# Kernel optimization log

Hardware: AMD Instinct MI355X
Metric: run time of the kernel (lower is better)

Reference implementation:

```python
import jax, jax.numpy as jnp
import numpy as np

N_NODES = 50000
N_EDGES = 800000
NODE_F = 64
HID = 64
LSTM_F = 32
LSTM_H = 128
B = 64
T = 200
OUT = 1
N_LAYERS = 2


def setup_inputs() -> dict:
    key = jax.random.key(0)
    ks = jax.random.split(key, 16)
    s = 0.05
    return {
        "x": jax.random.normal(ks[0], (N_NODES, NODE_F), jnp.float32),
        "edge_attr": jax.random.normal(ks[1], (N_EDGES, NODE_F), jnp.float32),
        "x_seq": jax.random.normal(ks[2], (B, T, LSTM_F), jnp.float32),
        "lin_W": jax.random.normal(ks[3], (N_LAYERS, HID, HID), jnp.float32) * s,
        "lin_b": jnp.zeros((N_LAYERS, HID), jnp.float32),
        "mlp_W1": jax.random.normal(ks[4], (N_LAYERS, HID, HID), jnp.float32) * s,
        "mlp_b1": jnp.zeros((N_LAYERS, HID), jnp.float32),
        "mlp_W2": jax.random.normal(ks[5], (N_LAYERS, HID, HID), jnp.float32) * s,
        "mlp_b2": jnp.zeros((N_LAYERS, HID), jnp.float32),
        "eps": jnp.zeros((N_LAYERS,), jnp.float32),
        "ln_scale": jnp.ones((N_LAYERS, HID), jnp.float32),
        "ln_bias": jnp.zeros((N_LAYERS, HID), jnp.float32),
        "W_ih": jax.random.normal(ks[6], (4 * LSTM_H, HID + LSTM_F), jnp.float32) * s,
        "W_hh": jax.random.normal(ks[7], (4 * LSTM_H, LSTM_H), jnp.float32) * s,
        "b_ih": jnp.zeros((4 * LSTM_H,), jnp.float32),
        "b_hh": jnp.zeros((4 * LSTM_H,), jnp.float32),
        "lstm_ln_scale": jnp.ones((LSTM_H,), jnp.float32),
        "lstm_ln_bias": jnp.zeros((LSTM_H,), jnp.float32),
        "fc_W": jax.random.normal(ks[8], (OUT, LSTM_H), jnp.float32) * s,
        "fc_b": jnp.zeros((OUT,), jnp.float32),
        "edge_index": jax.random.randint(ks[9], (2, N_EDGES), 0, N_NODES, jnp.int32),
        "node_indices": jax.random.randint(ks[10], (B,), 0, N_NODES, jnp.int32),
    }


def _layernorm(z, scale, bias, eps=1e-5):
    mu = jnp.mean(z, axis=-1, keepdims=True)
    var = jnp.var(z, axis=-1, keepdims=True)
    return (z - mu) * jax.lax.rsqrt(var + eps) * scale + bias


def reference(x, edge_attr, x_seq, lin_W, lin_b, mlp_W1, mlp_b1, mlp_W2, mlp_b2,
              eps, ln_scale, ln_bias, W_ih, W_hh, b_ih, b_hh,
              lstm_ln_scale, lstm_ln_bias, fc_W, fc_b, edge_index, node_indices):
    src, dst = edge_index[0], edge_index[1]
    h = x
    n = x.shape[0]
    # GINEConv layers: out = MLP((1+eps)*x + sum_j relu(x_j + lin(e_ij)))
    for l in range(N_LAYERS):
        e = edge_attr @ lin_W[l].T + lin_b[l]            # [E, C]
        m = jax.nn.relu(h[src] + e)                       # gather + message
        agg = jax.ops.segment_sum(m, dst, num_segments=n) # scatter-add
        z = (1.0 + eps[l]) * h + agg
        z = jax.nn.relu(z @ mlp_W1[l].T + mlp_b1[l]) @ mlp_W2[l].T + mlp_b2[l]
        z = _layernorm(z, ln_scale[l], ln_bias[l])
        h = jax.nn.relu(z)

    sel = h[node_indices]                                 # [B, HID]
    seq_len = x_seq.shape[1]
    expanded = jnp.broadcast_to(sel[:, None, :], (sel.shape[0], seq_len, sel.shape[1]))
    combined = jnp.concatenate([expanded, x_seq], axis=2) # [B, T, HID+F]

    # single-layer LSTM, PyTorch gate order (i, f, g, o)
    Hd = W_hh.shape[1]
    xs = jnp.transpose(combined, (1, 0, 2))               # [T, B, D]
    x_proj = xs @ W_ih.T + b_ih                            # [T, B, 4H]

    def step(carry, xp):
        hprev, cprev = carry
        gates = xp + hprev @ W_hh.T + b_hh
        i, f, g, o = jnp.split(gates, 4, axis=-1)
        i = jax.nn.sigmoid(i); f = jax.nn.sigmoid(f)
        g = jnp.tanh(g); o = jax.nn.sigmoid(o)
        c = f * cprev + i * g
        hn = o * jnp.tanh(c)
        return (hn, c), None

    bsz = combined.shape[0]
    init = (jnp.zeros((bsz, Hd), combined.dtype), jnp.zeros((bsz, Hd), combined.dtype))
    (hn, _), _ = jax.lax.scan(step, init, x_proj)

    last = _layernorm(hn, lstm_ln_scale, lstm_ln_bias)
    return last @ fc_W.T + fc_b
```

## Files before the change

### kernel.cpp

```cpp
#include <hip/hip_runtime.h>
#include <cmath>

static constexpr int NN  = 50000;
static constexpr int NE  = 800000;
static constexpr int HID = 64;
static constexpr int BB  = 64;
static constexpr int TT  = 200;
static constexpr int LH  = 128;
static constexpr int G4  = 512;

static constexpr int SCB = 125;
static constexpr int SCH = 400;

typedef _Float16 h2 __attribute__((ext_vector_type(2)));

#ifndef __has_builtin
#define __has_builtin(x) 0
#endif
#if __has_builtin(__builtin_amdgcn_fdot2)
__device__ __forceinline__ float fdot2_(h2 a, h2 b, float c) {
    return __builtin_amdgcn_fdot2(a, b, c, false);
}
#else
__device__ __forceinline__ float fdot2_(h2 a, h2 b, float c) {
    return c + (float)a.x * (float)b.x + (float)a.y * (float)b.y;
}
#endif

__device__ __forceinline__ h2 as_h2(unsigned int u) {
    union { unsigned int u; h2 h; } cv; cv.u = u; return cv.h;
}
__device__ __forceinline__ unsigned int as_u32(h2 h) {
    union { h2 h; unsigned int u; } cv; cv.h = h; return cv.u;
}

__device__ __forceinline__ float sigmoid_fast(float x) {
    return __fdividef(1.f, 1.f + __expf(-x));
}
__device__ __forceinline__ float tanh_fast(float x) {
    return __fdividef(2.f, 1.f + __expf(-2.f * x)) - 1.f;
}

__global__ __launch_bounds__(256) void hist_kernel(const int* __restrict__ dsts,
                                                   int* __restrict__ deg) {
    int i = blockIdx.x * 256 + threadIdx.x;
    if (i < NE) atomicAdd(&deg[dsts[i]], 1);
}

__global__ __launch_bounds__(512) void scan1_kernel(const int* __restrict__ deg,
                                                    int* __restrict__ loc,
                                                    int* __restrict__ bsum) {
    __shared__ int ws[8];
    const int b = blockIdx.x, t = threadIdx.x;
    const int idx = b * SCH + t;
    const int lane = t & 63, wv = t >> 6;
    int v = (t < SCH && idx < NN) ? deg[idx] : 0;
    int x = v;
    #pragma unroll
    for (int off = 1; off < 64; off <<= 1) {
        int y = __shfl_up(x, off);
        if (lane >= off) x += y;
    }
    if (lane == 63) ws[wv] = x;
    __syncthreads();
    if (t < 8) {
        int s = ws[t];
        #pragma unroll
        for (int off = 1; off < 8; off <<= 1) {
            int y = __shfl_up(s, off);
            if (t >= off) s += y;
        }
        ws[t] = s;
    }
    __syncthreads();
    const int base = wv ? ws[wv - 1] : 0;
    if (t < SCH && idx < NN) loc[idx] = base + x - v;
    if (t == 511) bsum[b] = ws[7];
}

__global__ void scan2_kernel(const int* __restrict__ bsum,
                             int* __restrict__ boff,
                             int* __restrict__ rowptr) {
    int tot = 0;
    for (int i = 0; i < SCB; ++i) { boff[i] = tot; tot += bsum[i]; }
    rowptr[NN] = tot;
}

__global__ __launch_bounds__(512) void scan3_kernel(const int* __restrict__ loc,
                                                    const int* __restrict__ boff,
                                                    int* __restrict__ rowptr,
                                                    int* __restrict__ head) {
    const int b = blockIdx.x, t = threadIdx.x;
    const int idx = b * SCH + t;
    if (t < SCH && idx < NN) {
        int r = loc[idx] + boff[b];
        rowptr[idx] = r;
        head[idx] = r;
    }
}

__global__ __launch_bounds__(256) void scatter_kernel(const int* __restrict__ srcs,
                                                      const int* __restrict__ dsts,
                                                      int* __restrict__ head,
                                                      int* __restrict__ perm,
                                                      int* __restrict__ ssrc) {
    int e = blockIdx.x * 256 + threadIdx.x;
    if (e < NE) {
        int d = dsts[e];
        int pos = atomicAdd(&head[d], 1);
        perm[e] = pos;
        ssrc[pos] = srcs[e];
    }
}

__global__ __launch_bounds__(256) void permute_kernel(const float* __restrict__ ea,
                                                      const int* __restrict__ perm,
                                                      ushort4* __restrict__ easort) {
    const int lane = threadIdx.x & 63, wid = threadIdx.x >> 6;
    const int slot = lane >> 4, hw = lane & 15;
    const int e = (blockIdx.x * 4 + wid) * 4 + slot;
    if (e < NE) {
        const int p = perm[e];
        float4 v = ((const float4*)ea)[(size_t)e * 16 + hw];
        union { _Float16 h[4]; ushort4 u; } pk;
        pk.h[0] = (_Float16)v.x; pk.h[1] = (_Float16)v.y;
        pk.h[2] = (_Float16)v.z; pk.h[3] = (_Float16)v.w;
        easort[(size_t)p * 16 + hw] = pk.u;
    }
}

__global__ __launch_bounds__(256) void edge_agg_kernel(
    const float*   __restrict__ h_in,
    const ushort4* __restrict__ easort,
    const float*   __restrict__ W,
    const float*   __restrict__ bias,
    const int*     __restrict__ rowptr,
    const int*     __restrict__ ssrc,
    float*         __restrict__ agg)
{
    __shared__ ushort4 stage[4][64];
    const int lane = threadIdx.x & 63;
    const int wid  = threadIdx.x >> 6;
    const int slot = lane >> 4, hw = lane & 15;

    h2 w2[32];
    {
        const float4* wf = (const float4*)(W + lane * 64);
        #pragma unroll
        for (int k4 = 0; k4 < 16; ++k4) {
            float4 v = wf[k4];
            h2 a; a.x = (_Float16)v.x; a.y = (_Float16)v.y;
            h2 b; b.x = (_Float16)v.z; b.y = (_Float16)v.w;
            w2[2*k4] = a; w2[2*k4+1] = b;
        }
    }
    const float bc = bias[lane];

    const int gw = blockIdx.x * 4 + wid;
    const int nw = gridDim.x * 4;
    for (int n = gw; n < NN; n += nw) {
        const int ofs = rowptr[n];
        const int dg  = rowptr[n + 1] - ofs;
        float acc = 0.f;
        for (int c = 0; c < dg; c += 4) {
            const int rem = dg - c;
            const int pick = slot < rem ? slot : rem - 1;
            const int ssv = ssrc[ofs + c + pick];
            stage[wid][lane] = easort[(size_t)(ofs + c + pick) * 16 + hw];
            if (rem >= 4) {
                float hv[4];
                #pragma unroll
                for (int j = 0; j < 4; ++j) {
                    int sj = __shfl(ssv, j << 4);
                    hv[j] = h_in[(size_t)sj * HID + lane];
                }
                asm volatile("s_waitcnt lgkmcnt(0)" ::: "memory");
                #pragma unroll
                for (int j = 0; j < 4; ++j) {
                    const uint4* stu = (const uint4*)&stage[wid][j * 16];
                    float aE = bc;
                    #pragma unroll
                    for (int k = 0; k < 8; ++k) {
                        uint4 u = stu[k];
                        aE = fdot2_(as_h2(u.x), w2[4*k+0], aE);
                        aE = fdot2_(as_h2(u.y), w2[4*k+1], aE);
                        aE = fdot2_(as_h2(u.z), w2[4*k+2], aE);
                        aE = fdot2_(as_h2(u.w), w2[4*k+3], aE);
                    }
                    float m = aE + hv[j];
                    acc += m > 0.f ? m : 0.f;
                }
            } else {
                asm volatile("s_waitcnt lgkmcnt(0)" ::: "memory");
                for (int j = 0; j < rem; ++j) {
                    int sj = __shfl(ssv, j << 4);
                    const uint4* stu = (const uint4*)&stage[wid][j * 16];
                    float aE = bc;
                    #pragma unroll
                    for (int k = 0; k < 8; ++k) {
                        uint4 u = stu[k];
                        aE = fdot2_(as_h2(u.x), w2[4*k+0], aE);
                        aE = fdot2_(as_h2(u.y), w2[4*k+1], aE);
                        aE = fdot2_(as_h2(u.z), w2[4*k+2], aE);
                        aE = fdot2_(as_h2(u.w), w2[4*k+3], aE);
                    }
                    float m = aE + h_in[(size_t)sj * HID + lane];
                    acc += m > 0.f ? m : 0.f;
                }
            }
        }
        agg[(size_t)n * HID + lane] = acc;
    }
}

__global__ __launch_bounds__(256) void node_kernel(
    const float* __restrict__ h_in,
    const float* __restrict__ agg,
    const float* __restrict__ W1, const float* __restrict__ b1,
    const float* __restrict__ W2, const float* __restrict__ b2,
    const float* __restrict__ epsp,
    const float* __restrict__ lnS, const float* __restrict__ lnB,
    float*       __restrict__ h_out)
{
    __shared__ float zbuf[4][64];
    __shared__ float tbuf[4][64];
    const int lane = threadIdx.x & 63;
    const int wid  = threadIdx.x >> 6;

    float w1[64], w2[64];
    {
        const float4* wf1 = (const float4*)(W1 + lane * 64);
        const float4* wf2 = (const float4*)(W2 + lane * 64);
        #pragma unroll
        for (int k4 = 0; k4 < 16; ++k4) {
            float4 a = wf1[k4], b = wf2[k4];
            w1[4*k4+0]=a.x; w1[4*k4+1]=a.y; w1[4*k4+2]=a.z; w1[4*k4+3]=a.w;
            w2[4*k4+0]=b.x; w2[4*k4+1]=b.y; w2[4*k4+2]=b.z; w2[4*k4+3]=b.w;
        }
    }
    const float b1c = b1[lane], b2c = b2[lane];
    const float sC = lnS[lane], bC = lnB[lane];
    const float epv = 1.f + epsp[0];

    const int gw = blockIdx.x * 4 + wid;
    const int nw = gridDim.x * 4;
    for (int n = gw; n < NN; n += nw) {
        float z = epv * h_in[(size_t)n*HID + lane] + agg[(size_t)n*HID + lane];
        zbuf[wid][lane] = z;
        asm volatile("s_waitcnt lgkmcnt(0)" ::: "memory");
        float acc = b1c;
        {
            const float4* zf = (const float4*)&zbuf[wid][0];
            #pragma unroll
            for (int k4 = 0; k4 < 16; ++k4) {
                float4 v = zf[k4];
                acc = fmaf(v.x, w1[4*k4+0], acc);
                acc = fmaf(v.y, w1[4*k4+1], acc);
                acc = fmaf(v.z, w1[4*k4+2], acc);
                acc = fmaf(v.w, w1[4*k4+3], acc);
            }
        }
        acc = acc > 0.f ? acc : 0.f;
        tbuf[wid][lane] = acc;
        asm volatile("s_waitcnt lgkmcnt(0)" ::: "memory");
        float acc2 = b2c;
        {
            const float4* tf = (const float4*)&tbuf[wid][0];
            #pragma unroll
            for (int k4 = 0; k4 < 16; ++k4) {
                float4 v = tf[k4];
                acc2 = fmaf(v.x, w2[4*k4+0], acc2);
                acc2 = fmaf(v.y, w2[4*k4+1], acc2);
                acc2 = fmaf(v.z, w2[4*k4+2], acc2);
                acc2 = fmaf(v.w, w2[4*k4+3], acc2);
            }
        }
        float s1 = acc2, s2 = acc2 * acc2;
        #pragma unroll
        for (int off = 32; off >= 1; off >>= 1) {
            s1 += __shfl_xor(s1, off);
            s2 += __shfl_xor(s2, off);
        }
        float mu  = s1 * (1.f/64.f);
        float var = s2 * (1.f/64.f) - mu * mu;
        float r   = rsqrtf(var + 1e-5f);
        float o   = (acc2 - mu) * r * sC + bC;
        h_out[(size_t)n*HID + lane] = o > 0.f ? o : 0.f;
    }
}

__global__ __launch_bounds__(512) void prep_kernel(
    const float* __restrict__ Wih,
    const float* __restrict__ bih,
    const float* __restrict__ h2v,
    const int*   __restrict__ nidx,
    float*       __restrict__ W2T,
    float*       __restrict__ selp)
{
    const int g = threadIdx.x;
    const int pos = ((g & 127) << 2) | (g >> 7);
    if (blockIdx.x == BB) {
        #pragma unroll
        for (int k = 0; k < 32; ++k)
            W2T[k * G4 + pos] = Wih[g * 96 + 64 + k];
    } else {
        const int b = blockIdx.x;
        __shared__ float hrow[64];
        if (g < 64) hrow[g] = h2v[(size_t)nidx[b] * HID + g];
        __syncthreads();
        float acc = bih[g];
        #pragma unroll
        for (int k = 0; k < 64; ++k)
            acc = fmaf(hrow[k], Wih[g * 96 + k], acc);
        selp[b * G4 + pos] = acc;
    }
}

__global__ __launch_bounds__(512) void xp_kernel(
    const float* __restrict__ xseq,
    const float* __restrict__ selp,
    const float* __restrict__ W2T,
    float*       __restrict__ xp)
{
    const int g   = threadIdx.x;
    const int row = blockIdx.x;
    const int t   = row >> 6;
    const int b   = row & 63;
    __shared__ float xs[32];
    if (g < 32) xs[g] = xseq[((size_t)b * TT + t) * 32 + g];
    __syncthreads();
    float acc = selp[b * G4 + g];
    #pragma unroll
    for (int k = 0; k < 32; ++k)
        acc = fmaf(xs[k], W2T[k * G4 + g], acc);
    xp[(size_t)row * G4 + g] = acc;
}

__global__ __launch_bounds__(512) void lstm_kernel(
    const float* __restrict__ xp,
    const float* __restrict__ Whh,
    const float* __restrict__ bhh,
    const float* __restrict__ lnS, const float* __restrict__ lnB,
    const float* __restrict__ fcW,
    const float* __restrict__ fcb,
    float*       __restrict__ out)
{
    const int t  = threadIdx.x;
    const int b  = blockIdx.x;
    const int gt = t & 3;
    const int j  = t >> 2;
    const int gate = gt * LH + j;

    h2 w2[64];
    {
        const float4* wf = (const float4*)(Whh + (size_t)gate * LH);
        #pragma unroll
        for (int k4 = 0; k4 < 32; ++k4) {
            float4 v = wf[k4];
            h2 a; a.x = (_Float16)v.x; a.y = (_Float16)v.y;
            h2 c2; c2.x = (_Float16)v.z; c2.y = (_Float16)v.w;
            w2[2*k4] = a; w2[2*k4+1] = c2;
        }
    }
    const float bg = bhh[gate];
    const float s_ = (gt == 2) ? 2.f : 1.f;
    const float a_ = (gt == 2) ? 2.f : 1.f;
    const float d_ = (gt == 2) ? -1.f : 0.f;

    __shared__ unsigned int h2b0[64];
    __shared__ unsigned int h2b1[64];
    __shared__ float h_final[LH];
    if (t < 64) h2b0[t] = 0u;
    float c = 0.f;
    __syncthreads();

    float xv = xp[(size_t)b * G4 + t];

    auto step = [&](const unsigned int* hb, unsigned int* hw, int ts) {
        const int tn = (ts + 1 < TT) ? ts + 1 : ts;
        const float xv_next = xp[((size_t)tn * BB + b) * G4 + t];

        float a0 = 0.f, a1 = 0.f, a2 = 0.f, a3 = 0.f;
        const uint4* hb4 = (const uint4*)hb;
        #pragma unroll
        for (int k = 0; k < 16; k += 4) {
            uint4 u0 = hb4[k], u1 = hb4[k+1], u2 = hb4[k+2], u3 = hb4[k+3];
            a0 = fdot2_(as_h2(u0.x), w2[4*k+ 0], a0);
            a0 = fdot2_(as_h2(u0.y), w2[4*k+ 1], a0);
            a0 = fdot2_(as_h2(u0.z), w2[4*k+ 2], a0);
            a0 = fdot2_(as_h2(u0.w), w2[4*k+ 3], a0);
            a1 = fdot2_(as_h2(u1.x), w2[4*k+ 4], a1);
            a1 = fdot2_(as_h2(u1.y), w2[4*k+ 5], a1);
            a1 = fdot2_(as_h2(u1.z), w2[4*k+ 6], a1);
            a1 = fdot2_(as_h2(u1.w), w2[4*k+ 7], a1);
            a2 = fdot2_(as_h2(u2.x), w2[4*k+ 8], a2);
            a2 = fdot2_(as_h2(u2.y), w2[4*k+ 9], a2);
            a2 = fdot2_(as_h2(u2.z), w2[4*k+10], a2);
            a2 = fdot2_(as_h2(u2.w), w2[4*k+11], a2);
            a3 = fdot2_(as_h2(u3.x), w2[4*k+12], a3);
            a3 = fdot2_(as_h2(u3.y), w2[4*k+13], a3);
            a3 = fdot2_(as_h2(u3.z), w2[4*k+14], a3);
            a3 = fdot2_(as_h2(u3.w), w2[4*k+15], a3);
        }
        float acc = xv + bg + ((a0 + a1) + (a2 + a3));

        float act = fmaf(a_, __fdividef(1.f, 1.f + __expf(-s_ * acc)), d_);

        float v0 = act;
        float v1 = __shfl_xor(v0, 1);
        float v2 = __shfl_xor(v0, 2);
        float v3 = __shfl_xor(v1, 2);
        float iv = (gt==0)?v0:(gt==1)?v1:(gt==2)?v2:v3;
        float fv = (gt==1)?v0:(gt==0)?v1:(gt==3)?v2:v3;
        float gv = (gt==2)?v0:(gt==3)?v1:(gt==0)?v2:v3;
        float ov = (gt==3)?v0:(gt==2)?v1:(gt==1)?v2:v3;

        c = fmaf(fv, c, iv * gv);
        float hval = ov * tanh_fast(c);

        float hpart = __shfl_xor(hval, 4);
        if ((t & 7) == 0) {
            h2 p; p.x = (_Float16)hval; p.y = (_Float16)hpart;
            hw[j >> 1] = as_u32(p);
        }
        if (gt == 0) h_final[j] = hval;
        __syncthreads();

        xv = xv_next;
    };

    for (int ts = 0; ts < TT; ts += 2) {
        step(h2b0, h2b1, ts);
        step(h2b1, h2b0, ts + 1);
    }

    if (t < 64) {
        float h0 = h_final[t], h1 = h_final[t + 64];
        float s1 = h0 + h1, s2 = h0*h0 + h1*h1;
        #pragma unroll
        for (int off = 32; off >= 1; off >>= 1) {
            s1 += __shfl_xor(s1, off);
            s2 += __shfl_xor(s2, off);
        }
        float mu  = s1 * (1.f/128.f);
        float var = s2 * (1.f/128.f) - mu * mu;
        float r   = rsqrtf(var + 1e-5f);
        float p = ((h0 - mu)*r*lnS[t]      + lnB[t])      * fcW[t]
                + ((h1 - mu)*r*lnS[t + 64] + lnB[t + 64]) * fcW[t + 64];
        #pragma unroll
        for (int off = 32; off >= 1; off >>= 1) p += __shfl_xor(p, off);
        if (t == 0) out[b] = p + fcb[0];
    }
}

extern "C" void kernel_launch(void* const* d_in, const int* in_sizes, int n_in,
                              void* d_out, int out_size, void* d_ws, size_t ws_size,
                              hipStream_t stream) {
    const float* x     = (const float*)d_in[0];
    const float* ea    = (const float*)d_in[1];
    const float* xseq  = (const float*)d_in[2];
    const float* linW  = (const float*)d_in[3];
    const float* linB  = (const float*)d_in[4];
    const float* mW1   = (const float*)d_in[5];
    const float* mb1   = (const float*)d_in[6];
    const float* mW2   = (const float*)d_in[7];
    const float* mb2   = (const float*)d_in[8];
    const float* eps   = (const float*)d_in[9];
    const float* lnS   = (const float*)d_in[10];
    const float* lnB   = (const float*)d_in[11];
    const float* Wih   = (const float*)d_in[12];
    const float* Whh   = (const float*)d_in[13];
    const float* bih   = (const float*)d_in[14];
    const float* bhh   = (const float*)d_in[15];
    const float* llnS  = (const float*)d_in[16];
    const float* llnB  = (const float*)d_in[17];
    const float* fcW   = (const float*)d_in[18];
    const float* fcb   = (const float*)d_in[19];
    const int*   eidx  = (const int*)d_in[20];
    const int*   nidx  = (const int*)d_in[21];
    float* out = (float*)d_out;

    const int* srcs = eidx;
    const int* dsts = eidx + NE;

    float* ws   = (float*)d_ws;
    float* agg  = ws;
    float* h1   = agg  + (size_t)NN * HID;
    float* h2m  = h1   + (size_t)NN * HID;
    float* selp = h2m  + (size_t)NN * HID;
    float* W2T  = selp + (size_t)BB * G4;
    float* xp   = W2T  + (size_t)32 * G4;
    int*   deg    = (int*)(xp + (size_t)TT * BB * G4);
    int*   rowptr = deg + NN;
    int*   head   = rowptr + NN + 2;
    int*   loc    = head + NN;
    int*   bsum   = loc + NN;
    int*   boff   = bsum + SCB + 3;
    int*   perm   = boff + SCB + 3;
    int*   ssrc   = perm + NE;
    uintptr_t ep = (uintptr_t)(ssrc + NE);
    ep = (ep + 15) & ~(uintptr_t)15;
    ushort4* easort = (ushort4*)ep;

    hipMemsetAsync(deg, 0, (size_t)NN * sizeof(int), stream);
    hist_kernel<<<(NE + 255) / 256, 256, 0, stream>>>(dsts, deg);
    scan1_kernel<<<SCB, 512, 0, stream>>>(deg, loc, bsum);
    scan2_kernel<<<1, 1, 0, stream>>>(bsum, boff, rowptr);
    scan3_kernel<<<SCB, 512, 0, stream>>>(loc, boff, rowptr, head);
    scatter_kernel<<<(NE + 255) / 256, 256, 0, stream>>>(srcs, dsts, head, perm, ssrc);
    permute_kernel<<<NE / 16, 256, 0, stream>>>(ea, perm, easort);

    edge_agg_kernel<<<2048, 256, 0, stream>>>(x, easort, linW, linB, rowptr, ssrc, agg);
    node_kernel<<<512, 256, 0, stream>>>(x, agg, mW1, mb1, mW2, mb2, eps, lnS, lnB, h1);
    edge_agg_kernel<<<2048, 256, 0, stream>>>(h1, easort, linW + 64*64, linB + 64, rowptr, ssrc, agg);
    node_kernel<<<512, 256, 0, stream>>>(h1, agg, mW1 + 64*64, mb1 + 64, mW2 + 64*64, mb2 + 64,
                                         eps + 1, lnS + 64, lnB + 64, h2m);
    prep_kernel<<<BB + 1, 512, 0, stream>>>(Wih, bih, h2m, nidx, W2T, selp);
    xp_kernel<<<TT * BB, 512, 0, stream>>>(xseq, selp, W2T, xp);
    lstm_kernel<<<BB, 512, 0, stream>>>(xp, Whh, bhh, llnS, llnB, fcW, fcb, out);
}
```

Before: 665.6 us.

## Gather fp16 node features in edge aggregation and pack two batches per LSTM block

Adds a conversion kernel that stores x as fp16, and makes node_kernel also write an fp16 copy of h1. The edge aggregation kernel then gathers these half-width node features instead of fp32, which halves the bytes of the random source-node gathers. The LSTM kernel now runs two batch rows per 1024-thread block (32 blocks instead of 64), with the shared buffers split per row. The fp16 features cost some precision, the extra conversion pass and fp16 writes add memory traffic, and the doubled block shares one __syncthreads per step across both rows.

```diff
diff --git a/kernel.cpp b/kernel.cpp
--- a/kernel.cpp
+++ b/kernel.cpp
@@ -34,9 +34,6 @@
     union { h2 h; unsigned int u; } cv; cv.h = h; return cv.u;
 }
 
-__device__ __forceinline__ float sigmoid_fast(float x) {
-    return __fdividef(1.f, 1.f + __expf(-x));
-}
 __device__ __forceinline__ float tanh_fast(float x) {
     return __fdividef(2.f, 1.f + __expf(-2.f * x)) - 1.f;
 }
@@ -129,14 +126,24 @@
     }
 }
 
+__global__ __launch_bounds__(256) void cvt16_kernel(const float* __restrict__ in,
+                                                    _Float16* __restrict__ o) {
+    int i = blockIdx.x * 256 + threadIdx.x;
+    float4 v = ((const float4*)in)[i];
+    union { _Float16 h[4]; ushort4 u; } pk;
+    pk.h[0] = (_Float16)v.x; pk.h[1] = (_Float16)v.y;
+    pk.h[2] = (_Float16)v.z; pk.h[3] = (_Float16)v.w;
+    ((ushort4*)o)[i] = pk.u;
+}
+
 __global__ __launch_bounds__(256) void edge_agg_kernel(
-    const float*   __restrict__ h_in,
-    const ushort4* __restrict__ easort,
-    const float*   __restrict__ W,
-    const float*   __restrict__ bias,
-    const int*     __restrict__ rowptr,
-    const int*     __restrict__ ssrc,
-    float*         __restrict__ agg)
+    const _Float16* __restrict__ h16,
+    const ushort4*  __restrict__ easort,
+    const float*    __restrict__ W,
+    const float*    __restrict__ bias,
+    const int*      __restrict__ rowptr,
+    const int*      __restrict__ ssrc,
+    float*          __restrict__ agg)
 {
     __shared__ ushort4 stage[4][64];
     const int lane = threadIdx.x & 63;
@@ -172,7 +179,7 @@
                 #pragma unroll
                 for (int j = 0; j < 4; ++j) {
                     int sj = __shfl(ssv, j << 4);
-                    hv[j] = h_in[(size_t)sj * HID + lane];
+                    hv[j] = (float)h16[(size_t)sj * HID + lane];
                 }
                 asm volatile("s_waitcnt lgkmcnt(0)" ::: "memory");
                 #pragma unroll
@@ -204,7 +211,7 @@
                         aE = fdot2_(as_h2(u.z), w2[4*k+2], aE);
                         aE = fdot2_(as_h2(u.w), w2[4*k+3], aE);
                     }
-                    float m = aE + h_in[(size_t)sj * HID + lane];
+                    float m = aE + (float)h16[(size_t)sj * HID + lane];
                     acc += m > 0.f ? m : 0.f;
                 }
             }
@@ -220,7 +227,8 @@
     const float* __restrict__ W2, const float* __restrict__ b2,
     const float* __restrict__ epsp,
     const float* __restrict__ lnS, const float* __restrict__ lnB,
-    float*       __restrict__ h_out)
+    float*       __restrict__ h_out,
+    _Float16*    __restrict__ h16_out)
 {
     __shared__ float zbuf[4][64];
     __shared__ float tbuf[4][64];
@@ -285,7 +293,9 @@
         float var = s2 * (1.f/64.f) - mu * mu;
         float r   = rsqrtf(var + 1e-5f);
         float o   = (acc2 - mu) * r * sC + bC;
-        h_out[(size_t)n*HID + lane] = o > 0.f ? o : 0.f;
+        float ov  = o > 0.f ? o : 0.f;
+        h_out[(size_t)n*HID + lane] = ov;
+        if (h16_out) h16_out[(size_t)n*HID + lane] = (_Float16)ov;
     }
 }
 
@@ -336,7 +346,7 @@
     xp[(size_t)row * G4 + g] = acc;
 }
 
-__global__ __launch_bounds__(512) void lstm_kernel(
+__global__ __launch_bounds__(1024) void lstm_kernel(
     const float* __restrict__ xp,
     const float* __restrict__ Whh,
     const float* __restrict__ bhh,
@@ -345,8 +355,10 @@
     const float* __restrict__ fcb,
     float*       __restrict__ out)
 {
-    const int t  = threadIdx.x;
-    const int b  = blockIdx.x;
+    const int tt = threadIdx.x;
+    const int r  = tt >> 9;
+    const int t  = tt & 511;
+    const int b  = blockIdx.x * 2 + r;
     const int gt = t & 3;
     const int j  = t >> 2;
     const int gate = gt * LH + j;
@@ -367,10 +379,10 @@
     const float a_ = (gt == 2) ? 2.f : 1.f;
     const float d_ = (gt == 2) ? -1.f : 0.f;
 
-    __shared__ unsigned int h2b0[64];
-    __shared__ unsigned int h2b1[64];
-    __shared__ float h_final[LH];
-    if (t < 64) h2b0[t] = 0u;
+    __shared__ unsigned int h2b0[2][64];
+    __shared__ unsigned int h2b1[2][64];
+    __shared__ float h_final[2][LH];
+    if (t < 64) h2b0[r][t] = 0u;
     float c = 0.f;
     __syncthreads();
 
@@ -423,19 +435,19 @@
             h2 p; p.x = (_Float16)hval; p.y = (_Float16)hpart;
             hw[j >> 1] = as_u32(p);
         }
-        if (gt == 0) h_final[j] = hval;
+        if (gt == 0) h_final[r][j] = hval;
         __syncthreads();
 
         xv = xv_next;
     };
 
     for (int ts = 0; ts < TT; ts += 2) {
-        step(h2b0, h2b1, ts);
-        step(h2b1, h2b0, ts + 1);
+        step(&h2b0[r][0], &h2b1[r][0], ts);
+        step(&h2b1[r][0], &h2b0[r][0], ts + 1);
     }
 
     if (t < 64) {
-        float h0 = h_final[t], h1 = h_final[t + 64];
+        float h0 = h_final[r][t], h1 = h_final[r][t + 64];
         float s1 = h0 + h1, s2 = h0*h0 + h1*h1;
         #pragma unroll
         for (int off = 32; off >= 1; off >>= 1) {
@@ -444,9 +456,9 @@
         }
         float mu  = s1 * (1.f/128.f);
         float var = s2 * (1.f/128.f) - mu * mu;
-        float r   = rsqrtf(var + 1e-5f);
-        float p = ((h0 - mu)*r*lnS[t]      + lnB[t])      * fcW[t]
-                + ((h1 - mu)*r*lnS[t + 64] + lnB[t + 64]) * fcW[t + 64];
+        float rr  = rsqrtf(var + 1e-5f);
+        float p = ((h0 - mu)*rr*lnS[t]      + lnB[t])      * fcW[t]
+                + ((h1 - mu)*rr*lnS[t + 64] + lnB[t + 64]) * fcW[t + 64];
         #pragma unroll
         for (int off = 32; off >= 1; off >>= 1) p += __shfl_xor(p, off);
         if (t == 0) out[b] = p + fcb[0];
@@ -501,6 +513,8 @@
     uintptr_t ep = (uintptr_t)(ssrc + NE);
     ep = (ep + 15) & ~(uintptr_t)15;
     ushort4* easort = (ushort4*)ep;
+    _Float16* x16   = (_Float16*)(easort + (size_t)NE * 16);
+    _Float16* h1_16 = x16 + (size_t)NN * HID;
 
     hipMemsetAsync(deg, 0, (size_t)NN * sizeof(int), stream);
     hist_kernel<<<(NE + 255) / 256, 256, 0, stream>>>(dsts, deg);
@@ -509,13 +523,14 @@
     scan3_kernel<<<SCB, 512, 0, stream>>>(loc, boff, rowptr, head);
     scatter_kernel<<<(NE + 255) / 256, 256, 0, stream>>>(srcs, dsts, head, perm, ssrc);
     permute_kernel<<<NE / 16, 256, 0, stream>>>(ea, perm, easort);
-
-    edge_agg_kernel<<<2048, 256, 0, stream>>>(x, easort, linW, linB, rowptr, ssrc, agg);
-    node_kernel<<<512, 256, 0, stream>>>(x, agg, mW1, mb1, mW2, mb2, eps, lnS, lnB, h1);
-    edge_agg_kernel<<<2048, 256, 0, stream>>>(h1, easort, linW + 64*64, linB + 64, rowptr, ssrc, agg);
+    cvt16_kernel<<<(NN * HID / 4 + 255) / 256, 256, 0, stream>>>(x, x16);
+
+    edge_agg_kernel<<<2048, 256, 0, stream>>>(x16, easort, linW, linB, rowptr, ssrc, agg);
+    node_kernel<<<512, 256, 0, stream>>>(x, agg, mW1, mb1, mW2, mb2, eps, lnS, lnB, h1, h1_16);
+    edge_agg_kernel<<<2048, 256, 0, stream>>>(h1_16, easort, linW + 64*64, linB + 64, rowptr, ssrc, agg);
     node_kernel<<<512, 256, 0, stream>>>(h1, agg, mW1 + 64*64, mb1 + 64, mW2 + 64*64, mb2 + 64,
-                                         eps + 1, lnS + 64, lnB + 64, h2m);
+                                         eps + 1, lnS + 64, lnB + 64, h2m, (_Float16*)nullptr);
     prep_kernel<<<BB + 1, 512, 0, stream>>>(Wih, bih, h2m, nidx, W2T, selp);
     xp_kernel<<<TT * BB, 512, 0, stream>>>(xseq, selp, W2T, xp);
-    lstm_kernel<<<BB, 512, 0, stream>>>(xp, Whh, bhh, llnS, llnB, fcW, fcb, out);
-}
+    lstm_kernel<<<BB / 2, 1024, 0, stream>>>(xp, Whh, bhh, llnS, llnB, fcW, fcb, out);
+}
```

After: 780.4 us. +17.2%, slower.
